# Performance work log

Hardware: AMD Instinct MI355X
Metric: run time of the kernel (lower is better)

Reference implementation:

```python
import jax, jax.numpy as jnp
import numpy as np

B, T, D, H = 2, 2048, 1024, 16
DH = D // H
EPS = 1e-3  # keras LayerNormalization default epsilon


def setup_inputs() -> dict:
    key = jax.random.key(0)
    ks = jax.random.split(key, 10)
    s = 1.0 / np.sqrt(D)
    return {
        "x": jax.random.normal(ks[0], (B, T, D), jnp.float32),
        "wq": jax.random.normal(ks[1], (D, D), jnp.float32) * s,
        "bq": jnp.zeros((D,), jnp.float32),
        "wk": jax.random.normal(ks[2], (D, D), jnp.float32) * s,
        "bk": jnp.zeros((D,), jnp.float32),
        "wv": jax.random.normal(ks[3], (D, D), jnp.float32) * s,
        "bv": jnp.zeros((D,), jnp.float32),
        "wo": jax.random.normal(ks[4], (D, D), jnp.float32) * s,
        "bo": jnp.zeros((D,), jnp.float32),
        "scale": jnp.asarray(1.0, jnp.float32),  # learnable scalar, init 1.0
        "gamma": jnp.ones((D,), jnp.float32),
        "beta": jnp.zeros((D,), jnp.float32),
    }


def _split_heads(t):
    # [B,T,D] -> [B,T,H,DH] -> [H,B,T,DH]; head h takes channels h*DH:(h+1)*DH,
    # matching tf.concat(tf.split(t, H, axis=-1), axis=0) up to batch layout.
    return t.reshape(B, T, H, DH).transpose(2, 0, 1, 3)


def reference(x, wq, bq, wk, bk, wv, bv, wo, bo, scale, gamma, beta):
    q = _split_heads(x @ wq + bq)  # [H,B,T,DH]
    k = _split_heads(x @ wk + bk)
    v = _split_heads(x @ wv + bv)
    scores = scale * jnp.einsum("hbqd,hbkd->hbqk", q, k)  # [H,B,Tq,Tk]
    attn = jax.nn.softmax(scores, axis=-1)
    ctx = jnp.einsum("hbqk,hbkd->hbqd", attn, v)  # [H,B,T,DH]
    # inverse of split: heads back to last dim in head order
    merged = ctx.transpose(1, 2, 0, 3).reshape(B, T, D)
    out = merged @ wo + bo
    out = out + x  # residual connection
    mean = jnp.mean(out, axis=-1, keepdims=True)
    var = jnp.var(out, axis=-1, keepdims=True)
    out = (out - mean) * jax.lax.rsqrt(var + EPS) * gamma + beta
    return out
```

## Files before the change

### kernel.cpp

```cpp
#include <hip/hip_runtime.h>
#include <hip/hip_bf16.h>

#define B_ 2
#define T_ 2048
#define D_ 1024
#define H_ 16
#define M_ (B_ * T_)

typedef __attribute__((ext_vector_type(4))) float f32x4;
typedef __attribute__((ext_vector_type(16))) float f32x16;
typedef __attribute__((ext_vector_type(8))) short s16x8;
typedef __attribute__((ext_vector_type(4))) short s16x4;
typedef __attribute__((ext_vector_type(4))) unsigned u32x4;

__device__ __forceinline__ short f2bs(float f) {
  unsigned u = __builtin_bit_cast(unsigned, f);
  u += 0x7fffu + ((u >> 16) & 1u);
  return (short)(u >> 16);
}
__device__ __forceinline__ unsigned cvt_pk_bf16(float lo, float hi) {
  unsigned r;
  asm("v_cvt_pk_bf16_f32 %0, %1, %2" : "=v"(r) : "v"(lo), "v"(hi));
  return r;
}
__device__ __forceinline__ void gl_lds16(const short* g, short* l) {
  __builtin_amdgcn_global_load_lds(
      (const __attribute__((address_space(1))) unsigned int*)g,
      (__attribute__((address_space(3))) unsigned int*)l, 16, 0, 0);
}

__global__ __launch_bounds__(256) void cvt_f32_bf16(const float* __restrict__ in,
                                                    short* __restrict__ out, int n4) {
  int i = blockIdx.x * 256 + threadIdx.x;
  if (i < n4) {
    float4 v = ((const float4*)in)[i];
    s16x4 o;
    o.x = f2bs(v.x); o.y = f2bs(v.y); o.z = f2bs(v.z); o.w = f2bs(v.w);
    ((s16x4*)out)[i] = o;
  }
}

__global__ __launch_bounds__(256) void cvt_transpose(
    const float* __restrict__ w0, const float* __restrict__ w1,
    const float* __restrict__ w2, const float* __restrict__ w3,
    short* __restrict__ o0, short* __restrict__ o1,
    short* __restrict__ o2, short* __restrict__ o3) {
  __shared__ float tile[64][65];
  const float* W; short* Wt;
  if (blockIdx.z == 0) { W = w0; Wt = o0; }
  else if (blockIdx.z == 1) { W = w1; Wt = o1; }
  else if (blockIdx.z == 2) { W = w2; Wt = o2; }
  else { W = w3; Wt = o3; }
  const int k0 = blockIdx.x * 64, n0 = blockIdx.y * 64;
  const int t = threadIdx.x;
  const int c = t & 63, r4 = t >> 6;
#pragma unroll
  for (int i = 0; i < 16; ++i) {
    int row = i * 4 + r4;
    tile[row][c] = W[(size_t)(k0 + row) * D_ + n0 + c];
  }
  __syncthreads();
#pragma unroll
  for (int i = 0; i < 16; ++i) {
    int row = i * 4 + r4;
    Wt[(size_t)(n0 + row) * D_ + k0 + c] = f2bs(tile[c][row]);
  }
}

template <int MODE>
__device__ __forceinline__ void gemm_core(short As[128][64], short Bs[128][64],
                                          const short* __restrict__ A,
                                          const short* __restrict__ Wt,
                                          const float* __restrict__ bias,
                                          const float* __restrict__ resid,
                                          void* __restrict__ outp, float mult) {
  const int t = threadIdx.x;
  const int lane = t & 63, wid = t >> 6;
  const int l15 = lane & 15, g = lane >> 4;
  const int wr = wid >> 1, wc = wid & 1;
  const int f = blockIdx.y * 8 + blockIdx.x;
  const int nf = (f & 7) * 32 + (f >> 3);
  const int n0 = (nf & 7) * 128;
  const int m0 = (nf >> 3) * 128;

  const f32x4 fz = {0.f, 0.f, 0.f, 0.f};
  f32x4 acc[4][4];
#pragma unroll
  for (int m = 0; m < 4; ++m)
#pragma unroll
    for (int n = 0; n < 4; ++n) acc[m][n] = fz;

  const int srw = lane >> 3;
  const int csw8 = ((lane & 7) ^ srw) * 8;
  const short* apg = A + (size_t)(m0 + wid * 32 + srw) * D_ + csw8;
  const short* bpg = Wt + (size_t)(n0 + wid * 32 + srw) * D_ + csw8;

  const int ch = ((g ^ (l15 & 7)) * 8);

  for (int k0 = 0; k0 < D_; k0 += 64) {
    __syncthreads();
#pragma unroll
    for (int i = 0; i < 4; ++i) {
      gl_lds16(apg + (size_t)i * 8 * D_ + k0, &As[wid * 32 + i * 8][0]);
      gl_lds16(bpg + (size_t)i * 8 * D_ + k0, &Bs[wid * 32 + i * 8][0]);
    }
    __syncthreads();
#pragma unroll
    for (int kk2 = 0; kk2 < 2; ++kk2) {
      const int x = kk2 * 32;
      s16x8 af[4], bfr[4];
#pragma unroll
      for (int m = 0; m < 4; ++m)
        af[m] = *(const s16x8*)&As[wr * 64 + m * 16 + l15][ch ^ x];
#pragma unroll
      for (int n = 0; n < 4; ++n)
        bfr[n] = *(const s16x8*)&Bs[wc * 64 + n * 16 + l15][ch ^ x];
#pragma unroll
      for (int m = 0; m < 4; ++m)
#pragma unroll
        for (int n = 0; n < 4; ++n)
          acc[m][n] = __builtin_amdgcn_mfma_f32_16x16x32_bf16(af[m], bfr[n], acc[m][n], 0, 0, 0);
    }
  }

#pragma unroll
  for (int m = 0; m < 4; ++m) {
#pragma unroll
    for (int n = 0; n < 4; ++n) {
      const int col = n0 + wc * 64 + n * 16 + l15;
      const float bv = bias[col];
#pragma unroll
      for (int i = 0; i < 4; ++i) {
        const int row = m0 + wr * 64 + m * 16 + g * 4 + i;
        float v = acc[m][n][i] + bv;
        if (MODE == 1) {
          ((float*)outp)[(size_t)row * D_ + col] = v + resid[(size_t)row * D_ + col];
        } else {
          ((short*)outp)[(size_t)row * D_ + col] = f2bs(v * mult);
        }
      }
    }
  }
}

__global__ __launch_bounds__(256) void gemm_qkv_kernel(
    const short* __restrict__ xb, const short* __restrict__ wq,
    const short* __restrict__ wk, const short* __restrict__ wv,
    const float* __restrict__ bq, const float* __restrict__ bk,
    const float* __restrict__ bv, const float* __restrict__ scale_p,
    short* __restrict__ Qb, short* __restrict__ Kb, short* __restrict__ Vb) {
  __shared__ __align__(16) short As[128][64];
  __shared__ __align__(16) short Bs[128][64];
  const short* W;
  const float* bias;
  short* out;
  float mult = 1.0f;
  if (blockIdx.z == 0) { W = wq; bias = bq; out = Qb; mult = scale_p[0] * 1.44269504f; }
  else if (blockIdx.z == 1) { W = wk; bias = bk; out = Kb; }
  else { W = wv; bias = bv; out = Vb; }
  gemm_core<0>(As, Bs, xb, W, bias, nullptr, out, mult);
}

__global__ __launch_bounds__(256) void gemm_out_kernel(
    const short* __restrict__ ctx, const short* __restrict__ wo,
    const float* __restrict__ bo, const float* __restrict__ x,
    float* __restrict__ out) {
  __shared__ __align__(16) short As[128][64];
  __shared__ __align__(16) short Bs[128][64];
  gemm_core<1>(As, Bs, ctx, wo, bo, x, out, 1.0f);
}

__global__ __launch_bounds__(128) void attn_kernel(
    const short* __restrict__ Qb, const short* __restrict__ Kb,
    const short* __restrict__ Vb, short* __restrict__ ctx) {
  __shared__ __align__(16) short Ks[64][64];
  __shared__ __align__(16) unsigned Vt[64][36];

  const int bid = blockIdx.x;
  const int xcd = bid & 7, slot = bid >> 3;
  const int grp = ((slot >> 4) << 3) | xcd;
  const int qt = slot & 15;
  const int h = grp >> 1, b = grp & 1;

  const int hc = h * 64;
  const size_t tokbase = (size_t)b * T_;
  const int t = threadIdx.x, lane = t & 63, w = t >> 6;
  const int l31 = lane & 31, hbit = lane >> 5;
  const int swz = (l31 & 7) << 3;

  s16x8 qf[2][4];
#pragma unroll
  for (int qg = 0; qg < 2; ++qg) {
    const short* qp =
        Qb + (tokbase + (size_t)(qt * 128 + w * 64 + qg * 32 + l31)) * D_ + hc + hbit * 8;
#pragma unroll
    for (int ks = 0; ks < 4; ++ks) qf[qg][ks] = *(const s16x8*)(qp + ks * 16);
  }

  const int krow = t >> 1, kcolb = (t & 1) * 32, kswz = (krow & 7) << 3;
  const int va = t & 31, vd0 = (t >> 5) * 16;
  const short* kp = Kb + (tokbase + krow) * D_ + hc + kcolb;
  const short* vp = Vb + (tokbase + 2 * (size_t)va) * D_ + hc + vd0;

  s16x8 kr[4], vA0, vA1, vB0, vB1;
#pragma unroll
  for (int c = 0; c < 4; ++c) kr[c] = *(const s16x8*)(kp + c * 8);
  vA0 = *(const s16x8*)vp;
  vA1 = *(const s16x8*)(vp + 8);
  vB0 = *(const s16x8*)(vp + D_);
  vB1 = *(const s16x8*)(vp + D_ + 8);

  f32x16 acc[2][2];
#pragma unroll
  for (int a = 0; a < 2; ++a)
#pragma unroll
    for (int b2 = 0; b2 < 2; ++b2)
#pragma unroll
      for (int i = 0; i < 16; ++i) acc[a][b2][i] = 0.f;
  float lsum[2] = {0.f, 0.f};

  const int NT = T_ / 64;
  for (int kt = 0; kt < NT; ++kt) {
    __syncthreads();
#pragma unroll
    for (int c = 0; c < 4; ++c)
      *(s16x8*)&Ks[krow][(kcolb + c * 8) ^ kswz] = kr[c];
    {
      u32x4 a0 = __builtin_bit_cast(u32x4, vA0), b0 = __builtin_bit_cast(u32x4, vB0);
      u32x4 a1 = __builtin_bit_cast(u32x4, vA1), b1 = __builtin_bit_cast(u32x4, vB1);
#pragma unroll
      for (int jd = 0; jd < 4; ++jd) {
        Vt[vd0 + 2 * jd][va] = __builtin_amdgcn_perm(b0[jd], a0[jd], 0x05040100u);
        Vt[vd0 + 2 * jd + 1][va] = __builtin_amdgcn_perm(b0[jd], a0[jd], 0x07060302u);
        Vt[vd0 + 8 + 2 * jd][va] = __builtin_amdgcn_perm(b1[jd], a1[jd], 0x05040100u);
        Vt[vd0 + 8 + 2 * jd + 1][va] = __builtin_amdgcn_perm(b1[jd], a1[jd], 0x07060302u);
      }
    }
    __syncthreads();
    if (kt + 1 < NT) {
      const short* kp2 = kp + (size_t)(kt + 1) * 64 * D_;
#pragma unroll
      for (int c = 0; c < 4; ++c) kr[c] = *(const s16x8*)(kp2 + c * 8);
      const short* vp2 = vp + (size_t)(kt + 1) * 64 * D_;
      vA0 = *(const s16x8*)vp2;
      vA1 = *(const s16x8*)(vp2 + 8);
      vB0 = *(const s16x8*)(vp2 + D_);
      vB1 = *(const s16x8*)(vp2 + D_ + 8);
    }

#pragma unroll
    for (int kb = 0; kb < 2; ++kb) {
      s16x8 kf[4];
#pragma unroll
      for (int ks = 0; ks < 4; ++ks)
        kf[ks] = *(const s16x8*)&Ks[kb * 32 + l31][(ks * 16 + hbit * 8) ^ swz];
      f32x16 S0, S1;
#pragma unroll
      for (int i = 0; i < 16; ++i) { S0[i] = 0.f; S1[i] = 0.f; }
#pragma unroll
      for (int ks = 0; ks < 4; ++ks) {
        S0 = __builtin_amdgcn_mfma_f32_32x32x16_bf16(kf[ks], qf[0][ks], S0, 0, 0, 0);
        S1 = __builtin_amdgcn_mfma_f32_32x32x16_bf16(kf[ks], qf[1][ks], S1, 0, 0, 0);
      }
      s16x8 pf[2][2];
#pragma unroll
      for (int qg = 0; qg < 2; ++qg) {
        const f32x16& S = qg ? S1 : S0;
        unsigned d[8];
        float ls = 0.f;
#pragma unroll
        for (int m = 0; m < 4; ++m) {
          float p0 = __builtin_amdgcn_exp2f(S[4 * m + 0]);
          float p1 = __builtin_amdgcn_exp2f(S[4 * m + 1]);
          float p2 = __builtin_amdgcn_exp2f(S[4 * m + 2]);
          float p3 = __builtin_amdgcn_exp2f(S[4 * m + 3]);
          ls += (p0 + p1) + (p2 + p3);
          d[m * 2 + 0] = cvt_pk_bf16(p0, p1);
          d[m * 2 + 1] = cvt_pk_bf16(p2, p3);
        }
        lsum[qg] += ls;
#pragma unroll
        for (int s2 = 0; s2 < 2; ++s2) {
          unsigned own0 = d[(2 * s2) * 2 + 0], own1 = d[(2 * s2) * 2 + 1];
          unsigned oth0 = d[(2 * s2 + 1) * 2 + 0], oth1 = d[(2 * s2 + 1) * 2 + 1];
          unsigned send0 = hbit ? own0 : oth0;
          unsigned send1 = hbit ? own1 : oth1;
          unsigned r0 = (unsigned)__shfl_xor((int)send0, 32);
          unsigned r1 = (unsigned)__shfl_xor((int)send1, 32);
          u32x4 bf;
          bf[0] = hbit ? r0 : own0;
          bf[1] = hbit ? r1 : own1;
          bf[2] = hbit ? oth0 : r0;
          bf[3] = hbit ? oth1 : r1;
          pf[qg][s2] = __builtin_bit_cast(s16x8, bf);
        }
      }
#pragma unroll
      for (int db = 0; db < 2; ++db) {
        s16x8 av0 = *(const s16x8*)&Vt[db * 32 + l31][kb * 16 + hbit * 4];
        s16x8 av1 = *(const s16x8*)&Vt[db * 32 + l31][kb * 16 + 8 + hbit * 4];
#pragma unroll
        for (int qg = 0; qg < 2; ++qg) {
          acc[db][qg] = __builtin_amdgcn_mfma_f32_32x32x16_bf16(av0, pf[qg][0], acc[db][qg], 0, 0, 0);
          acc[db][qg] = __builtin_amdgcn_mfma_f32_32x32x16_bf16(av1, pf[qg][1], acc[db][qg], 0, 0, 0);
        }
      }
    }
  }

#pragma unroll
  for (int qg = 0; qg < 2; ++qg) {
    lsum[qg] += __shfl_xor(lsum[qg], 32);
    float inv = 1.f / lsum[qg];
    const size_t token = tokbase + (size_t)(qt * 128 + w * 64 + qg * 32 + l31);
    short* cp = ctx + token * D_ + hc;
#pragma unroll
    for (int db = 0; db < 2; ++db) {
#pragma unroll
      for (int rq = 0; rq < 4; ++rq) {
        s16x4 o;
        o.x = f2bs(acc[db][qg][rq * 4 + 0] * inv);
        o.y = f2bs(acc[db][qg][rq * 4 + 1] * inv);
        o.z = f2bs(acc[db][qg][rq * 4 + 2] * inv);
        o.w = f2bs(acc[db][qg][rq * 4 + 3] * inv);
        *(s16x4*)(cp + db * 32 + rq * 8 + hbit * 4) = o;
      }
    }
  }
}

__global__ __launch_bounds__(256) void ln_kernel(float* __restrict__ out,
                                                 const float* __restrict__ gamma,
                                                 const float* __restrict__ beta) {
  __shared__ float reds[4], redss[4];
  const size_t row = blockIdx.x;
  float* p = out + row * D_;
  const int t = threadIdx.x;
  float4 v = ((const float4*)p)[t];
  float s = v.x + v.y + v.z + v.w;
  float ss = v.x * v.x + v.y * v.y + v.z * v.z + v.w * v.w;
#pragma unroll
  for (int off = 1; off < 64; off <<= 1) {
    s += __shfl_xor(s, off);
    ss += __shfl_xor(ss, off);
  }
  const int wid = t >> 6, lane = t & 63;
  if (lane == 0) { reds[wid] = s; redss[wid] = ss; }
  __syncthreads();
  float S = reds[0] + reds[1] + reds[2] + reds[3];
  float SS = redss[0] + redss[1] + redss[2] + redss[3];
  const float mean = S * (1.f / D_);
  const float var = SS * (1.f / D_) - mean * mean;
  const float r = rsqrtf(var + 1e-3f);
  float4 gm = ((const float4*)gamma)[t];
  float4 bt = ((const float4*)beta)[t];
  float4 o;
  o.x = (v.x - mean) * r * gm.x + bt.x;
  o.y = (v.y - mean) * r * gm.y + bt.y;
  o.z = (v.z - mean) * r * gm.z + bt.z;
  o.w = (v.w - mean) * r * gm.w + bt.w;
  ((float4*)p)[t] = o;
}

extern "C" void kernel_launch(void* const* d_in, const int* in_sizes, int n_in,
                              void* d_out, int out_size, void* d_ws, size_t ws_size,
                              hipStream_t stream) {
  const float* x = (const float*)d_in[0];
  const float* wq = (const float*)d_in[1];
  const float* bq = (const float*)d_in[2];
  const float* wk = (const float*)d_in[3];
  const float* bk = (const float*)d_in[4];
  const float* wv = (const float*)d_in[5];
  const float* bv = (const float*)d_in[6];
  const float* wo = (const float*)d_in[7];
  const float* bo = (const float*)d_in[8];
  const float* scale = (const float*)d_in[9];
  const float* gamma = (const float*)d_in[10];
  const float* beta = (const float*)d_in[11];
  float* out = (float*)d_out;

  short* xb = (short*)d_ws;
  short* wqt = xb + (size_t)M_ * D_;
  short* wkt = wqt + (size_t)D_ * D_;
  short* wvt = wkt + (size_t)D_ * D_;
  short* wot = wvt + (size_t)D_ * D_;
  short* Qb = wot + (size_t)D_ * D_;
  short* Kb = Qb + (size_t)M_ * D_;
  short* Vb = Kb + (size_t)M_ * D_;
  short* ctx = Vb + (size_t)M_ * D_;

  const int n4x = M_ * D_ / 4;
  cvt_f32_bf16<<<dim3((n4x + 255) / 256), 256, 0, stream>>>(x, xb, n4x);
  cvt_transpose<<<dim3(16, 16, 4), 256, 0, stream>>>(wq, wk, wv, wo, wqt, wkt, wvt, wot);

  gemm_qkv_kernel<<<dim3(D_ / 128, M_ / 128, 3), 256, 0, stream>>>(
      xb, wqt, wkt, wvt, bq, bk, bv, scale, Qb, Kb, Vb);

  attn_kernel<<<dim3(512), 128, 0, stream>>>(Qb, Kb, Vb, ctx);

  gemm_out_kernel<<<dim3(D_ / 128, M_ / 128), 256, 0, stream>>>(ctx, wot, bo, x, out);

  ln_kernel<<<dim3(M_), 256, 0, stream>>>(out, gamma, beta);
}
```

Measured before the change: 137.6 us.

## Split attention over two key halves and merge partials in a combine kernel

The attention grid is doubled: each block now handles half of the keys for its query tile. It writes unnormalized bf16 partial outputs into two buffers, reusing the xb and ctx scratch space, and stores per-row softmax sums into the now-free weight scratch. A new combine kernel adds the two partials and divides by the total sum. The aim is better occupancy on the GPU, since 512 blocks of 128 threads underfill the device. The cost is an extra launch, extra global traffic, and extra rounding from storing unnormalized partials in bf16.

New measurement: 146.3 us. +6.3%, slower.

```diff
diff --git a/kernel.cpp b/kernel.cpp
--- a/kernel.cpp
+++ b/kernel.cpp
@@ -17,6 +17,9 @@
   unsigned u = __builtin_bit_cast(unsigned, f);
   u += 0x7fffu + ((u >> 16) & 1u);
   return (short)(u >> 16);
+}
+__device__ __forceinline__ float bs2f(short s) {
+  return __builtin_bit_cast(float, ((unsigned)(unsigned short)s) << 16);
 }
 __device__ __forceinline__ unsigned cvt_pk_bf16(float lo, float hi) {
   unsigned r;
@@ -172,18 +175,21 @@
 
 __global__ __launch_bounds__(128) void attn_kernel(
     const short* __restrict__ Qb, const short* __restrict__ Kb,
-    const short* __restrict__ Vb, short* __restrict__ ctx) {
+    const short* __restrict__ Vb, short* __restrict__ Oa,
+    short* __restrict__ Ob, float* __restrict__ lsums) {
   __shared__ __align__(16) short Ks[64][64];
   __shared__ __align__(16) unsigned Vt[64][36];
 
   const int bid = blockIdx.x;
   const int xcd = bid & 7, slot = bid >> 3;
-  const int grp = ((slot >> 4) << 3) | xcd;
-  const int qt = slot & 15;
+  const int grp = ((slot >> 5) << 3) | xcd;
+  const int within = slot & 31;
+  const int qt = within & 15, split = within >> 4;
   const int h = grp >> 1, b = grp & 1;
 
   const int hc = h * 64;
   const size_t tokbase = (size_t)b * T_;
+  const size_t keybase = tokbase + (size_t)split * (T_ / 2);
   const int t = threadIdx.x, lane = t & 63, w = t >> 6;
   const int l31 = lane & 31, hbit = lane >> 5;
   const int swz = (l31 & 7) << 3;
@@ -199,8 +205,8 @@
 
   const int krow = t >> 1, kcolb = (t & 1) * 32, kswz = (krow & 7) << 3;
   const int va = t & 31, vd0 = (t >> 5) * 16;
-  const short* kp = Kb + (tokbase + krow) * D_ + hc + kcolb;
-  const short* vp = Vb + (tokbase + 2 * (size_t)va) * D_ + hc + vd0;
+  const short* kp = Kb + (keybase + krow) * D_ + hc + kcolb;
+  const short* vp = Vb + (keybase + 2 * (size_t)va) * D_ + hc + vd0;
 
   s16x8 kr[4], vA0, vA1, vB0, vB1;
 #pragma unroll
@@ -219,7 +225,7 @@
       for (int i = 0; i < 16; ++i) acc[a][b2][i] = 0.f;
   float lsum[2] = {0.f, 0.f};
 
-  const int NT = T_ / 64;
+  const int NT = (T_ / 2) / 64;
   for (int kt = 0; kt < NT; ++kt) {
     __syncthreads();
 #pragma unroll
@@ -308,25 +314,43 @@
     }
   }
 
+  short* Op = split ? Ob : Oa;
 #pragma unroll
   for (int qg = 0; qg < 2; ++qg) {
     lsum[qg] += __shfl_xor(lsum[qg], 32);
-    float inv = 1.f / lsum[qg];
     const size_t token = tokbase + (size_t)(qt * 128 + w * 64 + qg * 32 + l31);
-    short* cp = ctx + token * D_ + hc;
+    if (hbit == 0) lsums[(size_t)split * M_ * H_ + token * H_ + h] = lsum[qg];
+    short* cp = Op + token * D_ + hc;
 #pragma unroll
     for (int db = 0; db < 2; ++db) {
 #pragma unroll
       for (int rq = 0; rq < 4; ++rq) {
         s16x4 o;
-        o.x = f2bs(acc[db][qg][rq * 4 + 0] * inv);
-        o.y = f2bs(acc[db][qg][rq * 4 + 1] * inv);
-        o.z = f2bs(acc[db][qg][rq * 4 + 2] * inv);
-        o.w = f2bs(acc[db][qg][rq * 4 + 3] * inv);
+        o.x = f2bs(acc[db][qg][rq * 4 + 0]);
+        o.y = f2bs(acc[db][qg][rq * 4 + 1]);
+        o.z = f2bs(acc[db][qg][rq * 4 + 2]);
+        o.w = f2bs(acc[db][qg][rq * 4 + 3]);
         *(s16x4*)(cp + db * 32 + rq * 8 + hbit * 4) = o;
       }
     }
   }
+}
+
+__global__ __launch_bounds__(256) void combine_kernel(
+    const short* __restrict__ Oa, short* __restrict__ Oc,
+    const float* __restrict__ lsums) {
+  const int i = blockIdx.x * 256 + threadIdx.x;
+  const int token = i >> 7;
+  const int h = (i & 127) >> 3;
+  const float la = lsums[(size_t)token * H_ + h];
+  const float lb = lsums[(size_t)M_ * H_ + (size_t)token * H_ + h];
+  const float rinv = 1.f / (la + lb);
+  s16x8 a = ((const s16x8*)Oa)[i];
+  s16x8 b = ((const s16x8*)Oc)[i];
+  s16x8 o;
+#pragma unroll
+  for (int j = 0; j < 8; ++j) o[j] = f2bs((bs2f(a[j]) + bs2f(b[j])) * rinv);
+  ((s16x8*)Oc)[i] = o;
 }
 
 __global__ __launch_bounds__(256) void ln_kernel(float* __restrict__ out,
@@ -388,6 +412,7 @@
   short* Kb = Qb + (size_t)M_ * D_;
   short* Vb = Kb + (size_t)M_ * D_;
   short* ctx = Vb + (size_t)M_ * D_;
+  float* lsums = (float*)wqt;
 
   const int n4x = M_ * D_ / 4;
   cvt_f32_bf16<<<dim3((n4x + 255) / 256), 256, 0, stream>>>(x, xb, n4x);
@@ -396,7 +421,8 @@
   gemm_qkv_kernel<<<dim3(D_ / 128, M_ / 128, 3), 256, 0, stream>>>(
       xb, wqt, wkt, wvt, bq, bk, bv, scale, Qb, Kb, Vb);
 
-  attn_kernel<<<dim3(512), 128, 0, stream>>>(Qb, Kb, Vb, ctx);
+  attn_kernel<<<dim3(1024), 128, 0, stream>>>(Qb, Kb, Vb, xb, ctx, lsums);
+  combine_kernel<<<dim3(M_ * D_ / 8 / 256), 256, 0, stream>>>(xb, ctx, lsums);
 
   gemm_out_kernel<<<dim3(D_ / 128, M_ / 128), 256, 0, stream>>>(ctx, wot, bo, x, out);
 
```
